# Performance work log

Measured on AMD Instinct MI355X. Metric: run time of the kernel, lower is better.

The kernel has to match this reference:

```python
import jax, jax.numpy as jnp
import numpy as np

B, R, L, H = 2, 64, 512, 1024
NH_TOTAL = 16
NH = NH_TOTAL // 2          # 8 heads (config.num_attention_heads // 2)
HD = H // NH_TOTAL          # 64 head dim
AH = NH * HD                # 512 all_head_size


def setup_inputs() -> dict:
    key = jax.random.key(0)
    ks = jax.random.split(key, 8)
    hidden_states = jax.random.normal(ks[0], (B, R, L, H), jnp.float32)
    # RoFormer-style sinusoidal positions: [sin | cos] halves along last dim
    pos = np.arange(L, dtype=np.float32)[:, None]
    inv_freq = 1.0 / (10000.0 ** (np.arange(HD // 2, dtype=np.float32) * 2.0 / HD))
    ang = pos * inv_freq[None, :]                       # [L, HD//2]
    sinusoidal_pos = jnp.asarray(
        np.concatenate([np.sin(ang), np.cos(ang)], axis=-1), jnp.float32
    ).reshape(1, 1, L, HD)                               # broadcast vs [B,NH,L,HD]
    s = 0.02
    Wq = jax.random.normal(ks[1], (AH, H), jnp.float32) * s
    bq = jnp.zeros((AH,), jnp.float32)
    Wk = jax.random.normal(ks[2], (AH, H), jnp.float32) * s
    bk = jnp.zeros((AH,), jnp.float32)
    Wv = jax.random.normal(ks[3], (AH, H), jnp.float32) * s
    bv = jnp.zeros((AH,), jnp.float32)
    return {"hidden_states": hidden_states, "sinusoidal_pos": sinusoidal_pos,
            "Wq": Wq, "bq": bq, "Wk": Wk, "bk": bk, "Wv": Wv, "bv": bv}


def _rotate_half(x):
    # stack([-x_odd, x_even], -1).reshape_as(x)
    return jnp.stack([-x[..., 1::2], x[..., ::2]], axis=-1).reshape(x.shape)


def _apply_rope(x, sin_pos, cos_pos):
    return x * cos_pos + _rotate_half(x) * sin_pos


def reference(hidden_states, sinusoidal_pos, Wq, bq, Wk, bk, Wv, bv):
    b, r, l, h = hidden_states.shape

    def to_heads(x):  # [..., l, AH] -> [..., NH, l, HD]
        return x.reshape(*x.shape[:-1], NH, HD).swapaxes(-2, -3)

    # query/key only from row 0 ("star" attention); value from all rows
    row0 = hidden_states[:, 0]                               # [B, L, H]
    q = to_heads(row0 @ Wq.T + bq)                           # [B, NH, L, HD]
    k = to_heads(row0 @ Wk.T + bk)                           # [B, NH, L, HD]
    v = to_heads(hidden_states @ Wv.T + bv)                  # [B, R, NH, L, HD]

    sin, cos = jnp.split(sinusoidal_pos, 2, axis=-1)         # [1,1,L,HD//2] each
    sin_pos = jnp.stack([sin, sin], axis=-1).reshape(sinusoidal_pos.shape)
    cos_pos = jnp.stack([cos, cos], axis=-1).reshape(sinusoidal_pos.shape)
    q = _apply_rope(q, sin_pos, cos_pos)
    k = _apply_rope(k, sin_pos, cos_pos)

    scores = jnp.einsum('bnqd,bnkd->bnqk', q, k) / jnp.sqrt(jnp.float32(HD))
    probs = jax.nn.softmax(scores, axis=-1)                  # [B, NH, L, L]
    ctx = jnp.einsum('bnqk,brnkd->brnqd', probs, v)          # [B, R, NH, L, HD]
    ctx = ctx.swapaxes(-2, -3).reshape(b, r, l, AH)          # [B, R, L, AH]
    return ctx
```

## Files before the change

### kernel.cpp

```cpp
#include <hip/hip_runtime.h>
#include <math.h>

typedef __attribute__((ext_vector_type(8))) short short8;
typedef __attribute__((ext_vector_type(4))) float floatx4;

__device__ __forceinline__ unsigned int pack2_trunc(float a, float b) {
  return (__float_as_uint(a) >> 16) | (__float_as_uint(b) & 0xffff0000u);
}
__device__ __forceinline__ unsigned short f2bf_rne(float x) {
  unsigned int u = __float_as_uint(x);
  u += 0x7fff + ((u >> 16) & 1);
  return (unsigned short)(u >> 16);
}
__device__ __forceinline__ float bflo(unsigned int u) { return __uint_as_float(u << 16); }
__device__ __forceinline__ float bfhi(unsigned int u) { return __uint_as_float(u & 0xffff0000u); }

__global__ __launch_bounds__(256) void wcast_kernel(
    const float* __restrict__ W, unsigned short* __restrict__ Wb)
{
  size_t i = (size_t)blockIdx.x * 256 + threadIdx.x;
  const float4* p = (const float4*)(W + i * 8);
  float4 a0 = p[0], a1 = p[1];
  uint4 w;
  w.x = pack2_trunc(a0.x, a0.y); w.y = pack2_trunc(a0.z, a0.w);
  w.z = pack2_trunc(a1.x, a1.y); w.w = pack2_trunc(a1.z, a1.w);
  *(uint4*)&Wb[i * 8] = w;
}

__global__ __launch_bounds__(256, 2) void qk_proj_kernel(
    const float* __restrict__ hid,
    const float* __restrict__ Wq, const float* __restrict__ bq,
    const float* __restrict__ Wk, const float* __restrict__ bk,
    unsigned short* __restrict__ Qr, unsigned short* __restrict__ Kr)
{
  const float* W = blockIdx.z ? Wk : Wq;
  const float* bias = blockIdx.z ? bk : bq;
  unsigned short* out = blockIdx.z ? Kr : Qr;

  __shared__ unsigned short As[128][72];
  __shared__ unsigned short Bs[128][72];
  const int tid = threadIdx.x;
  const int m0 = blockIdx.y * 128;
  const int n0 = blockIdx.x * 128;
  const int bidx = m0 >> 9;
  const int l0 = m0 & 511;
  const float* Abase = hid + ((size_t)bidx * 32768 + l0) * 1024;
  const float* Bbase = W + (size_t)n0 * 1024;

  const int srow = tid >> 1;
  const int shalf = (tid & 1) * 32;
  const int lane = tid & 63;
  const int wave = tid >> 6;
  const int wm = (wave >> 1) * 64, wn = (wave & 1) * 64;
  const int mr = lane & 15, kq = lane >> 4;

  floatx4 acc[4][4];
#pragma unroll
  for (int i = 0; i < 4; ++i)
#pragma unroll
    for (int j = 0; j < 4; ++j) acc[i][j] = (floatx4){0.f, 0.f, 0.f, 0.f};

  for (int k0 = 0; k0 < 1024; k0 += 64) {
    const float4* ap = (const float4*)(Abase + (size_t)srow * 1024 + k0 + shalf);
    const float4* bp = (const float4*)(Bbase + (size_t)srow * 1024 + k0 + shalf);
#pragma unroll
    for (int j = 0; j < 4; ++j) {
      float4 a0 = ap[2 * j], a1 = ap[2 * j + 1];
      float4 b0 = bp[2 * j], b1 = bp[2 * j + 1];
      uint4 wa, wb;
      wa.x = pack2_trunc(a0.x, a0.y); wa.y = pack2_trunc(a0.z, a0.w);
      wa.z = pack2_trunc(a1.x, a1.y); wa.w = pack2_trunc(a1.z, a1.w);
      wb.x = pack2_trunc(b0.x, b0.y); wb.y = pack2_trunc(b0.z, b0.w);
      wb.z = pack2_trunc(b1.x, b1.y); wb.w = pack2_trunc(b1.z, b1.w);
      *(uint4*)&As[srow][shalf + j * 8] = wa;
      *(uint4*)&Bs[srow][shalf + j * 8] = wb;
    }
    __syncthreads();
#pragma unroll
    for (int ks = 0; ks < 2; ++ks) {
      short8 af[4], bfr[4];
#pragma unroll
      for (int i = 0; i < 4; ++i)
        af[i] = *(const short8*)&As[wm + i * 16 + mr][ks * 32 + kq * 8];
#pragma unroll
      for (int i = 0; i < 4; ++i)
        bfr[i] = *(const short8*)&Bs[wn + i * 16 + mr][ks * 32 + kq * 8];
#pragma unroll
      for (int i = 0; i < 4; ++i)
#pragma unroll
        for (int j = 0; j < 4; ++j)
          acc[i][j] = __builtin_amdgcn_mfma_f32_16x16x32_bf16(af[i], bfr[j], acc[i][j], 0, 0, 0);
    }
    __syncthreads();
  }

#pragma unroll
  for (int j = 0; j < 4; ++j) {
    int gn = n0 + wn + j * 16 + mr;
    float bb = bias[gn];
#pragma unroll
    for (int i = 0; i < 4; ++i) {
      int gm = m0 + wm + i * 16 + kq * 4;
      floatx4 a = acc[i][j];
#pragma unroll
      for (int rg = 0; rg < 4; ++rg)
        out[(size_t)(gm + rg) * 512 + gn] = f2bf_rne(a[rg] + bb);
    }
  }
}

__global__ __launch_bounds__(256, 2) void scores_softmax_kernel(
    const unsigned short* __restrict__ Qr,
    const unsigned short* __restrict__ Kr,
    const float* __restrict__ sinu,
    unsigned short* __restrict__ probs)
{
  __shared__ unsigned int KsL[512][34];
  __shared__ float Qs[8][64];
  const int tid = threadIdx.x;
  const int bn = blockIdx.y;
  const int b = bn >> 3, h = bn & 7;
  const int q0 = blockIdx.x * 8;

  for (int it = tid; it < 4096; it += 256) {
    int k = it >> 3, c = it & 7;
    uint4 v = *(const uint4*)(Kr + ((size_t)b * 512 + k) * 512 + h * 64 + c * 8);
    unsigned int uu[4] = {v.x, v.y, v.z, v.w};
#pragma unroll
    for (int p = 0; p < 4; ++p) {
      int i = c * 4 + p;
      float x0 = bflo(uu[p]), x1 = bfhi(uu[p]);
      float sn = sinu[k * 64 + i], cs = sinu[k * 64 + 32 + i];
      KsL[k][i] = pack2_trunc(x0 * cs - x1 * sn, x1 * cs + x0 * sn);
    }
  }
  if (tid < 64) {
    int q = tid >> 3, c = tid & 7;
    int gq = q0 + q;
    uint4 v = *(const uint4*)(Qr + ((size_t)b * 512 + gq) * 512 + h * 64 + c * 8);
    unsigned int uu[4] = {v.x, v.y, v.z, v.w};
#pragma unroll
    for (int p = 0; p < 4; ++p) {
      int i = c * 4 + p;
      float x0 = bflo(uu[p]), x1 = bfhi(uu[p]);
      float sn = sinu[gq * 64 + i], cs = sinu[gq * 64 + 32 + i];
      Qs[q][2 * i] = (x0 * cs - x1 * sn) * 0.125f;
      Qs[q][2 * i + 1] = (x1 * cs + x0 * sn) * 0.125f;
    }
  }
  __syncthreads();

  const int q = tid >> 5, kg = tid & 31;
  float qreg[64];
#pragma unroll
  for (int d = 0; d < 64; ++d) qreg[d] = Qs[q][d];

  float s[16];
#pragma unroll
  for (int j = 0; j < 16; ++j) {
    int kk = kg + 32 * j;
    float a = 0.f;
#pragma unroll
    for (int c = 0; c < 16; ++c) {
      uint2 u = *(const uint2*)&KsL[kk][2 * c];
      a += qreg[4 * c + 0] * bflo(u.x);
      a += qreg[4 * c + 1] * bfhi(u.x);
      a += qreg[4 * c + 2] * bflo(u.y);
      a += qreg[4 * c + 3] * bfhi(u.y);
    }
    s[j] = a;
  }
  float mx = s[0];
#pragma unroll
  for (int j = 1; j < 16; ++j) mx = fmaxf(mx, s[j]);
#pragma unroll
  for (int off = 1; off < 32; off <<= 1) mx = fmaxf(mx, __shfl_xor(mx, off));
  float sum = 0.f;
#pragma unroll
  for (int j = 0; j < 16; ++j) { s[j] = __expf(s[j] - mx); sum += s[j]; }
#pragma unroll
  for (int off = 1; off < 32; off <<= 1) sum += __shfl_xor(sum, off);
  float inv = 1.0f / sum;
  unsigned short* prow = probs + ((size_t)bn * 512 + (q0 + q)) * 512;
#pragma unroll
  for (int j = 0; j < 16; ++j) prow[kg + 32 * j] = f2bf_rne(s[j] * inv);
}

__global__ __launch_bounds__(512, 1) void vproj_kernel(
    const float* __restrict__ hid, const unsigned short* __restrict__ Wvb,
    const float* __restrict__ bv, unsigned short* __restrict__ VT)
{
  __shared__ unsigned short As[128][72];
  __shared__ unsigned short Bs[512][72];
  const int tid = threadIdx.x;
  const int m0 = blockIdx.x * 128;
  const float* Abase = hid + (size_t)m0 * 1024;

  const int lane = tid & 63;
  const int wave = tid >> 6;
  const int wm = (wave >> 2) * 64, wn = (wave & 3) * 128;
  const int mr = lane & 15, kq = lane >> 4;

  const int arow = tid >> 2, aseg = tid & 3;
  const int brow = tid >> 3, bchunk = tid & 7;

  floatx4 acc[4][8];
#pragma unroll
  for (int i = 0; i < 4; ++i)
#pragma unroll
    for (int j = 0; j < 8; ++j) acc[i][j] = (floatx4){0.f, 0.f, 0.f, 0.f};

  for (int k0 = 0; k0 < 1024; k0 += 64) {
    const float4* ap = (const float4*)(Abase + (size_t)arow * 1024 + k0 + aseg * 16);
    float4 a0 = ap[0], a1 = ap[1], a2 = ap[2], a3 = ap[3];
    uint4 w0, w1;
    w0.x = pack2_trunc(a0.x, a0.y); w0.y = pack2_trunc(a0.z, a0.w);
    w0.z = pack2_trunc(a1.x, a1.y); w0.w = pack2_trunc(a1.z, a1.w);
    w1.x = pack2_trunc(a2.x, a2.y); w1.y = pack2_trunc(a2.z, a2.w);
    w1.z = pack2_trunc(a3.x, a3.y); w1.w = pack2_trunc(a3.z, a3.w);
    *(uint4*)&As[arow][aseg * 16] = w0;
    *(uint4*)&As[arow][aseg * 16 + 8] = w1;
#pragma unroll
    for (int j = 0; j < 8; ++j) {
      int r = brow + j * 64;
      uint4 v = *(const uint4*)(Wvb + (size_t)r * 1024 + k0 + bchunk * 8);
      *(uint4*)&Bs[r][bchunk * 8] = v;
    }
    __syncthreads();
#pragma unroll
    for (int ks = 0; ks < 2; ++ks) {
      short8 af[4], bfr[8];
#pragma unroll
      for (int i = 0; i < 4; ++i)
        af[i] = *(const short8*)&As[wm + i * 16 + mr][ks * 32 + kq * 8];
#pragma unroll
      for (int j = 0; j < 8; ++j)
        bfr[j] = *(const short8*)&Bs[wn + j * 16 + mr][ks * 32 + kq * 8];
#pragma unroll
      for (int i = 0; i < 4; ++i)
#pragma unroll
        for (int j = 0; j < 8; ++j)
          acc[i][j] = __builtin_amdgcn_mfma_f32_16x16x32_bf16(af[i], bfr[j], acc[i][j], 0, 0, 0);
    }
    __syncthreads();
  }

  const int bidx = m0 >> 15;
  const int rr = (m0 >> 9) & 63;
  const int l0 = m0 & 511;
#pragma unroll
  for (int j = 0; j < 8; ++j) {
    int gn = wn + j * 16 + mr;
    int hh = gn >> 6, dd = gn & 63;
    float bb = bv[gn];
    size_t colbase = ((size_t)(bidx * 8 + hh) * 4096 + rr * 64 + dd) * 512;
#pragma unroll
    for (int i = 0; i < 4; ++i) {
      int gl = l0 + wm + i * 16 + kq * 4;
      floatx4 a = acc[i][j];
      uint2 pk;
      pk.x = (unsigned int)f2bf_rne(a[0] + bb) | ((unsigned int)f2bf_rne(a[1] + bb) << 16);
      pk.y = (unsigned int)f2bf_rne(a[2] + bb) | ((unsigned int)f2bf_rne(a[3] + bb) << 16);
      *(uint2*)&VT[colbase + gl] = pk;
    }
  }
}

__global__ __launch_bounds__(256, 2) void ctx_kernel(
    const unsigned short* __restrict__ probs,
    const unsigned short* __restrict__ VT,
    float* __restrict__ out)
{
  __shared__ unsigned short As[128][72];
  __shared__ unsigned short Bs[128][72];
  const int tid = threadIdx.x;
  const int n0 = blockIdx.x * 128;
  const int m0 = blockIdx.y * 128;
  const int z = blockIdx.z;
  const unsigned short* Ab = probs + (size_t)z * 512 * 512;
  const unsigned short* Bb = VT + (size_t)z * 4096 * 512;

  const int srow = tid >> 1;
  const int shalf = (tid & 1) * 32;
  const int lane = tid & 63;
  const int wave = tid >> 6;
  const int wm = (wave >> 1) * 64, wn = (wave & 1) * 64;
  const int mr = lane & 15, kq = lane >> 4;

  floatx4 acc[4][4];
#pragma unroll
  for (int i = 0; i < 4; ++i)
#pragma unroll
    for (int j = 0; j < 4; ++j) acc[i][j] = (floatx4){0.f, 0.f, 0.f, 0.f};

  for (int k0 = 0; k0 < 512; k0 += 64) {
    const uint4* ap = (const uint4*)(Ab + (size_t)(m0 + srow) * 512 + k0 + shalf);
    const uint4* bp = (const uint4*)(Bb + (size_t)(n0 + srow) * 512 + k0 + shalf);
#pragma unroll
    for (int j = 0; j < 4; ++j) {
      *(uint4*)&As[srow][shalf + j * 8] = ap[j];
      *(uint4*)&Bs[srow][shalf + j * 8] = bp[j];
    }
    __syncthreads();
#pragma unroll
    for (int ks = 0; ks < 2; ++ks) {
      short8 af[4], bfr[4];
#pragma unroll
      for (int i = 0; i < 4; ++i)
        af[i] = *(const short8*)&As[wm + i * 16 + mr][ks * 32 + kq * 8];
#pragma unroll
      for (int i = 0; i < 4; ++i)
        bfr[i] = *(const short8*)&Bs[wn + i * 16 + mr][ks * 32 + kq * 8];
#pragma unroll
      for (int i = 0; i < 4; ++i)
#pragma unroll
        for (int j = 0; j < 4; ++j)
          acc[i][j] = __builtin_amdgcn_mfma_f32_16x16x32_bf16(af[i], bfr[j], acc[i][j], 0, 0, 0);
    }
    __syncthreads();
  }

  const int bz = z >> 3, hh = z & 7;
#pragma unroll
  for (int j = 0; j < 4; ++j) {
    int gn = n0 + wn + j * 16 + mr;
    int rr = gn >> 6, dd = gn & 63;
    size_t colbase = (size_t)(bz * 64 + rr) * 262144 + hh * 64 + dd;
#pragma unroll
    for (int i = 0; i < 4; ++i) {
      int gq = m0 + wm + i * 16 + kq * 4;
      floatx4 a = acc[i][j];
#pragma unroll
      for (int rg = 0; rg < 4; ++rg)
        out[colbase + (size_t)(gq + rg) * 512] = a[rg];
    }
  }
}

extern "C" void kernel_launch(void* const* d_in, const int* in_sizes, int n_in,
                              void* d_out, int out_size, void* d_ws, size_t ws_size,
                              hipStream_t stream) {
  const float* hid  = (const float*)d_in[0];
  const float* sinu = (const float*)d_in[1];
  const float* Wq = (const float*)d_in[2];
  const float* bq = (const float*)d_in[3];
  const float* Wk = (const float*)d_in[4];
  const float* bk = (const float*)d_in[5];
  const float* Wv = (const float*)d_in[6];
  const float* bv = (const float*)d_in[7];
  float* out = (float*)d_out;

  char* ws = (char*)d_ws;
  unsigned short* Qr = (unsigned short*)(ws);
  unsigned short* Kr = (unsigned short*)(ws + (1u << 20));
  unsigned short* probs = (unsigned short*)(ws + (2u << 20));
  unsigned short* Wvb = (unsigned short*)(ws + (10u << 20));
  unsigned short* VT = (unsigned short*)(ws + (16u << 20));

  wcast_kernel<<<dim3(256), 256, 0, stream>>>(Wv, Wvb);
  qk_proj_kernel<<<dim3(4, 8, 2), 256, 0, stream>>>(hid, Wq, bq, Wk, bk, Qr, Kr);
  scores_softmax_kernel<<<dim3(64, 16), 256, 0, stream>>>(Qr, Kr, sinu, probs);
  vproj_kernel<<<dim3(512), 512, 0, stream>>>(hid, Wvb, bv, VT);
  ctx_kernel<<<dim3(32, 4, 16), 256, 0, stream>>>(probs, VT, out);
}
```

Baseline: 632.8 us.

## Use MFMA for scores, stream Wv from global in vproj, stage ctx stores

The scores/softmax kernel now computes Q·K^T with bf16 MFMA over 64 query rows per block, keeping RoPE-rotated Q (pre-scaled and rounded to bf16) in registers, and launches 8x fewer blocks. The V projection drops the shared-memory B tile, reads Wv fragments straight from global/L2, and double-buffers the converted activation tile so loads overlap MFMA, raising occupancy to two blocks per CU. The ctx kernel routes its output through a shared-memory tile so it can write coalesced float4 rows instead of strided scalar stores. These changes raise register and global-load pressure, and Q now loses some precision from the bf16 rounding.

After: 644.5 us. About the same (+1.8%).

```diff
diff --git a/kernel.cpp b/kernel.cpp
--- a/kernel.cpp
+++ b/kernel.cpp
@@ -115,94 +115,103 @@
     const float* __restrict__ sinu,
     unsigned short* __restrict__ probs)
 {
-  __shared__ unsigned int KsL[512][34];
-  __shared__ float Qs[8][64];
+  __shared__ unsigned short Ks[512][72];
   const int tid = threadIdx.x;
   const int bn = blockIdx.y;
   const int b = bn >> 3, h = bn & 7;
-  const int q0 = blockIdx.x * 8;
+  const int q0 = blockIdx.x * 64;
+  const int lane = tid & 63, wave = tid >> 6;
+  const int mr = lane & 15, kq = lane >> 4;
 
   for (int it = tid; it < 4096; it += 256) {
     int k = it >> 3, c = it & 7;
     uint4 v = *(const uint4*)(Kr + ((size_t)b * 512 + k) * 512 + h * 64 + c * 8);
     unsigned int uu[4] = {v.x, v.y, v.z, v.w};
+    unsigned int res[4];
 #pragma unroll
     for (int p = 0; p < 4; ++p) {
       int i = c * 4 + p;
       float x0 = bflo(uu[p]), x1 = bfhi(uu[p]);
       float sn = sinu[k * 64 + i], cs = sinu[k * 64 + 32 + i];
-      KsL[k][i] = pack2_trunc(x0 * cs - x1 * sn, x1 * cs + x0 * sn);
-    }
-  }
-  if (tid < 64) {
-    int q = tid >> 3, c = tid & 7;
-    int gq = q0 + q;
-    uint4 v = *(const uint4*)(Qr + ((size_t)b * 512 + gq) * 512 + h * 64 + c * 8);
+      res[p] = pack2_trunc(x0 * cs - x1 * sn, x1 * cs + x0 * sn);
+    }
+    uint4 w; w.x = res[0]; w.y = res[1]; w.z = res[2]; w.w = res[3];
+    *(uint4*)&Ks[k][c * 8] = w;
+  }
+
+  const int gq_load = q0 + wave * 16 + mr;
+  short8 aq[2];
+#pragma unroll
+  for (int ks = 0; ks < 2; ++ks) {
+    int d0 = ks * 32 + kq * 8;
+    uint4 v = *(const uint4*)(Qr + ((size_t)b * 512 + gq_load) * 512 + h * 64 + d0);
     unsigned int uu[4] = {v.x, v.y, v.z, v.w};
+    union { short8 s; unsigned short u[8]; } r;
 #pragma unroll
     for (int p = 0; p < 4; ++p) {
-      int i = c * 4 + p;
+      int i = (d0 >> 1) + p;
       float x0 = bflo(uu[p]), x1 = bfhi(uu[p]);
-      float sn = sinu[gq * 64 + i], cs = sinu[gq * 64 + 32 + i];
-      Qs[q][2 * i] = (x0 * cs - x1 * sn) * 0.125f;
-      Qs[q][2 * i + 1] = (x1 * cs + x0 * sn) * 0.125f;
-    }
+      float sn = sinu[gq_load * 64 + i], cs = sinu[gq_load * 64 + 32 + i];
+      r.u[2 * p]     = f2bf_rne((x0 * cs - x1 * sn) * 0.125f);
+      r.u[2 * p + 1] = f2bf_rne((x1 * cs + x0 * sn) * 0.125f);
+    }
+    aq[ks] = r.s;
   }
   __syncthreads();
 
-  const int q = tid >> 5, kg = tid & 31;
-  float qreg[64];
-#pragma unroll
-  for (int d = 0; d < 64; ++d) qreg[d] = Qs[q][d];
-
-  float s[16];
-#pragma unroll
-  for (int j = 0; j < 16; ++j) {
-    int kk = kg + 32 * j;
-    float a = 0.f;
-#pragma unroll
-    for (int c = 0; c < 16; ++c) {
-      uint2 u = *(const uint2*)&KsL[kk][2 * c];
-      a += qreg[4 * c + 0] * bflo(u.x);
-      a += qreg[4 * c + 1] * bfhi(u.x);
-      a += qreg[4 * c + 2] * bflo(u.y);
-      a += qreg[4 * c + 3] * bfhi(u.y);
-    }
-    s[j] = a;
-  }
-  float mx = s[0];
-#pragma unroll
-  for (int j = 1; j < 16; ++j) mx = fmaxf(mx, s[j]);
-#pragma unroll
-  for (int off = 1; off < 32; off <<= 1) mx = fmaxf(mx, __shfl_xor(mx, off));
-  float sum = 0.f;
-#pragma unroll
-  for (int j = 0; j < 16; ++j) { s[j] = __expf(s[j] - mx); sum += s[j]; }
-#pragma unroll
-  for (int off = 1; off < 32; off <<= 1) sum += __shfl_xor(sum, off);
-  float inv = 1.0f / sum;
-  unsigned short* prow = probs + ((size_t)bn * 512 + (q0 + q)) * 512;
-#pragma unroll
-  for (int j = 0; j < 16; ++j) prow[kg + 32 * j] = f2bf_rne(s[j] * inv);
-}
-
-__global__ __launch_bounds__(512, 1) void vproj_kernel(
+  floatx4 acc[32];
+#pragma unroll
+  for (int j = 0; j < 32; ++j) acc[j] = (floatx4){0.f, 0.f, 0.f, 0.f};
+#pragma unroll
+  for (int j = 0; j < 32; ++j) {
+    short8 b0 = *(const short8*)&Ks[j * 16 + mr][kq * 8];
+    short8 b1 = *(const short8*)&Ks[j * 16 + mr][32 + kq * 8];
+    acc[j] = __builtin_amdgcn_mfma_f32_16x16x32_bf16(aq[0], b0, acc[j], 0, 0, 0);
+    acc[j] = __builtin_amdgcn_mfma_f32_16x16x32_bf16(aq[1], b1, acc[j], 0, 0, 0);
+  }
+
+  float mx[4] = {-1e30f, -1e30f, -1e30f, -1e30f};
+#pragma unroll
+  for (int j = 0; j < 32; ++j)
+#pragma unroll
+    for (int rg = 0; rg < 4; ++rg) mx[rg] = fmaxf(mx[rg], acc[j][rg]);
+#pragma unroll
+  for (int rg = 0; rg < 4; ++rg)
+#pragma unroll
+    for (int off = 1; off < 16; off <<= 1) mx[rg] = fmaxf(mx[rg], __shfl_xor(mx[rg], off));
+  float sum[4] = {0.f, 0.f, 0.f, 0.f};
+#pragma unroll
+  for (int j = 0; j < 32; ++j)
+#pragma unroll
+    for (int rg = 0; rg < 4; ++rg) {
+      float e = __expf(acc[j][rg] - mx[rg]);
+      acc[j][rg] = e; sum[rg] += e;
+    }
+#pragma unroll
+  for (int rg = 0; rg < 4; ++rg)
+#pragma unroll
+    for (int off = 1; off < 16; off <<= 1) sum[rg] += __shfl_xor(sum[rg], off);
+#pragma unroll
+  for (int rg = 0; rg < 4; ++rg) {
+    float inv = 1.0f / sum[rg];
+    unsigned short* prow = probs + ((size_t)bn * 512 + q0 + wave * 16 + kq * 4 + rg) * 512;
+#pragma unroll
+    for (int j = 0; j < 32; ++j) prow[j * 16 + mr] = f2bf_rne(acc[j][rg] * inv);
+  }
+}
+
+__global__ __launch_bounds__(512, 2) void vproj_kernel(
     const float* __restrict__ hid, const unsigned short* __restrict__ Wvb,
     const float* __restrict__ bv, unsigned short* __restrict__ VT)
 {
-  __shared__ unsigned short As[128][72];
-  __shared__ unsigned short Bs[512][72];
+  __shared__ unsigned short As[2][128][72];
   const int tid = threadIdx.x;
   const int m0 = blockIdx.x * 128;
   const float* Abase = hid + (size_t)m0 * 1024;
-
-  const int lane = tid & 63;
-  const int wave = tid >> 6;
+  const int lane = tid & 63, wave = tid >> 6;
   const int wm = (wave >> 2) * 64, wn = (wave & 3) * 128;
   const int mr = lane & 15, kq = lane >> 4;
-
   const int arow = tid >> 2, aseg = tid & 3;
-  const int brow = tid >> 3, bchunk = tid & 7;
 
   floatx4 acc[4][8];
 #pragma unroll
@@ -210,39 +219,54 @@
 #pragma unroll
     for (int j = 0; j < 8; ++j) acc[i][j] = (floatx4){0.f, 0.f, 0.f, 0.f};
 
-  for (int k0 = 0; k0 < 1024; k0 += 64) {
-    const float4* ap = (const float4*)(Abase + (size_t)arow * 1024 + k0 + aseg * 16);
+  const unsigned short* Bl = Wvb + (size_t)(wn + mr) * 1024 + kq * 8;
+  const float* aptr = Abase + (size_t)arow * 1024 + aseg * 16;
+
+  {
+    const float4* ap = (const float4*)aptr;
     float4 a0 = ap[0], a1 = ap[1], a2 = ap[2], a3 = ap[3];
     uint4 w0, w1;
     w0.x = pack2_trunc(a0.x, a0.y); w0.y = pack2_trunc(a0.z, a0.w);
     w0.z = pack2_trunc(a1.x, a1.y); w0.w = pack2_trunc(a1.z, a1.w);
     w1.x = pack2_trunc(a2.x, a2.y); w1.y = pack2_trunc(a2.z, a2.w);
     w1.z = pack2_trunc(a3.x, a3.y); w1.w = pack2_trunc(a3.z, a3.w);
-    *(uint4*)&As[arow][aseg * 16] = w0;
-    *(uint4*)&As[arow][aseg * 16 + 8] = w1;
-#pragma unroll
-    for (int j = 0; j < 8; ++j) {
-      int r = brow + j * 64;
-      uint4 v = *(const uint4*)(Wvb + (size_t)r * 1024 + k0 + bchunk * 8);
-      *(uint4*)&Bs[r][bchunk * 8] = v;
-    }
-    __syncthreads();
+    *(uint4*)&As[0][arow][aseg * 16] = w0;
+    *(uint4*)&As[0][arow][aseg * 16 + 8] = w1;
+  }
+  int cur = 0;
+  for (int t = 0; t < 16; ++t) {
+    const int k0 = t * 64;
+    __syncthreads();
+    float4 a0, a1, a2, a3;
+    if (t < 15) {
+      const float4* ap = (const float4*)(aptr + k0 + 64);
+      a0 = ap[0]; a1 = ap[1]; a2 = ap[2]; a3 = ap[3];
+    }
 #pragma unroll
     for (int ks = 0; ks < 2; ++ks) {
       short8 af[4], bfr[8];
 #pragma unroll
       for (int i = 0; i < 4; ++i)
-        af[i] = *(const short8*)&As[wm + i * 16 + mr][ks * 32 + kq * 8];
+        af[i] = *(const short8*)&As[cur][wm + i * 16 + mr][ks * 32 + kq * 8];
 #pragma unroll
       for (int j = 0; j < 8; ++j)
-        bfr[j] = *(const short8*)&Bs[wn + j * 16 + mr][ks * 32 + kq * 8];
+        bfr[j] = *(const short8*)(Bl + (size_t)j * 16384 + k0 + ks * 32);
 #pragma unroll
       for (int i = 0; i < 4; ++i)
 #pragma unroll
         for (int j = 0; j < 8; ++j)
           acc[i][j] = __builtin_amdgcn_mfma_f32_16x16x32_bf16(af[i], bfr[j], acc[i][j], 0, 0, 0);
     }
-    __syncthreads();
+    if (t < 15) {
+      uint4 w0, w1;
+      w0.x = pack2_trunc(a0.x, a0.y); w0.y = pack2_trunc(a0.z, a0.w);
+      w0.z = pack2_trunc(a1.x, a1.y); w0.w = pack2_trunc(a1.z, a1.w);
+      w1.x = pack2_trunc(a2.x, a2.y); w1.y = pack2_trunc(a2.z, a2.w);
+      w1.z = pack2_trunc(a3.x, a3.y); w1.w = pack2_trunc(a3.z, a3.w);
+      *(uint4*)&As[cur ^ 1][arow][aseg * 16] = w0;
+      *(uint4*)&As[cur ^ 1][arow][aseg * 16 + 8] = w1;
+      cur ^= 1;
+    }
   }
 
   const int bidx = m0 >> 15;
@@ -273,6 +297,7 @@
 {
   __shared__ unsigned short As[128][72];
   __shared__ unsigned short Bs[128][72];
+  __shared__ float Cf[32][132];
   const int tid = threadIdx.x;
   const int n0 = blockIdx.x * 128;
   const int m0 = blockIdx.y * 128;
@@ -321,19 +346,27 @@
   }
 
   const int bz = z >> 3, hh = z & 7;
-#pragma unroll
-  for (int j = 0; j < 4; ++j) {
-    int gn = n0 + wn + j * 16 + mr;
-    int rr = gn >> 6, dd = gn & 63;
-    size_t colbase = (size_t)(bz * 64 + rr) * 262144 + hh * 64 + dd;
-#pragma unroll
-    for (int i = 0; i < 4; ++i) {
-      int gq = m0 + wm + i * 16 + kq * 4;
+  const int lrw = (wave >> 1) * 16 + kq * 4;
+  const int lr2 = tid >> 3, seg = tid & 7;
+  const int gqb = m0 + (lr2 >> 4) * 64 + (lr2 & 15);
+  const int gn2 = n0 + seg * 16;
+  const int rr2 = gn2 >> 6, dd2 = gn2 & 63;
+  float* obase = out + (size_t)(bz * 64 + rr2) * 262144 + hh * 64 + dd2;
+#pragma unroll
+  for (int i = 0; i < 4; ++i) {
+    __syncthreads();
+#pragma unroll
+    for (int j = 0; j < 4; ++j) {
       floatx4 a = acc[i][j];
-#pragma unroll
-      for (int rg = 0; rg < 4; ++rg)
-        out[colbase + (size_t)(gq + rg) * 512] = a[rg];
-    }
+      int col = wn + j * 16 + mr;
+#pragma unroll
+      for (int rg = 0; rg < 4; ++rg) Cf[lrw + rg][col] = a[rg];
+    }
+    __syncthreads();
+    float* op = obase + (size_t)(gqb + i * 16) * 512;
+#pragma unroll
+    for (int e = 0; e < 4; ++e)
+      *(float4*)&op[e * 4] = *(const float4*)&Cf[lr2][seg * 16 + e * 4];
   }
 }
 
@@ -359,7 +392,7 @@
 
   wcast_kernel<<<dim3(256), 256, 0, stream>>>(Wv, Wvb);
   qk_proj_kernel<<<dim3(4, 8, 2), 256, 0, stream>>>(hid, Wq, bq, Wk, bk, Qr, Kr);
-  scores_softmax_kernel<<<dim3(64, 16), 256, 0, stream>>>(Qr, Kr, sinu, probs);
+  scores_softmax_kernel<<<dim3(8, 16), 256, 0, stream>>>(Qr, Kr, sinu, probs);
   vproj_kernel<<<dim3(512), 512, 0, stream>>>(hid, Wvb, bv, VT);
   ctx_kernel<<<dim3(32, 4, 16), 256, 0, stream>>>(probs, VT, out);
 }
```
